# Kernel tuning notes

Measured on AMD Instinct MI355X. Metric: run time of the kernel, lower is better.

Reference implementation:

```python
import jax, jax.numpy as jnp
import numpy as np

N = 131072      # atoms
NB = 8192       # blocks (~16 atoms each)
H = 256         # hidden_size
NH = 8          # num_heads
HD = H // NH
RBF = 16
HQ = H // 4
CUTOFF = 10.0
EPS = 1e-5


def _ln(x, g, b):
    mu = jnp.mean(x, axis=-1, keepdims=True)
    var = jnp.var(x, axis=-1, keepdims=True)
    return (x - mu) * jax.lax.rsqrt(var + EPS) * g + b


def setup_inputs():
    key = jax.random.key(0)
    ks = jax.random.split(key, 20)
    w = lambda k, sh: jax.random.normal(k, sh, jnp.float32) * 0.02
    z = lambda d: jnp.zeros((d,), jnp.float32)
    return {
        'atom_features': jax.random.normal(ks[0], (N, H), jnp.float32),
        'atom_positions': jax.random.uniform(ks[1], (N, 3), jnp.float32) * 20.0,
        'block_id': jnp.arange(N, dtype=jnp.int32) // (N // NB),
        'inter_edges': jax.random.randint(ks[2], (2, 4 * NB), 0, NB, jnp.int32),
        'pma_seed': w(ks[3], (H,)),
        'pma_wq': w(ks[4], (H, H)), 'pma_bq': z(H),
        'pma_wk': w(ks[5], (H, H)), 'pma_bk': z(H),
        'pma_wv': w(ks[6], (H, H)), 'pma_bv': z(H),
        'pma_wo': w(ks[7], (H, H)), 'pma_bo': z(H),
        'centers': jnp.linspace(0.0, CUTOFF, RBF, dtype=jnp.float32),
        'widths': jnp.full((RBF,), CUTOFF / RBF, jnp.float32),
        'geom_w': w(ks[8], (RBF, HQ)), 'geom_b': z(HQ),
        'cq_w': w(ks[9], (H, H)), 'cq_b': z(H),
        'ck_w': w(ks[10], (H + HQ, H)), 'ck_b': z(H),
        'cv_w': w(ks[11], (H + HQ, H)), 'cv_b': z(H),
        'cmlp_w1': w(ks[12], (H, H)), 'cmlp_b1': z(H),
        'cmlp_w2': w(ks[13], (H, H)), 'cmlp_b2': z(H),
        'ffn_w1': w(ks[14], (H, 2 * H)), 'ffn_b1': z(2 * H),
        'ffn_w2': w(ks[15], (2 * H, H)), 'ffn_b2': z(H),
        'ln1_g': jnp.ones((H,), jnp.float32), 'ln1_b': z(H),
        'ln2_g': jnp.ones((H,), jnp.float32), 'ln2_b': z(H),
    }


def reference(atom_features, atom_positions, block_id, inter_edges,
              pma_seed, pma_wq, pma_bq, pma_wk, pma_bk, pma_wv, pma_bv, pma_wo, pma_bo,
              centers, widths, geom_w, geom_b, cq_w, cq_b, ck_w, ck_b, cv_w, cv_b,
              cmlp_w1, cmlp_b1, cmlp_w2, cmlp_b2, ffn_w1, ffn_b1, ffn_w2, ffn_b2,
              ln1_g, ln1_b, ln2_g, ln2_b):
    bid = block_id
    seg_sum = lambda x: jax.ops.segment_sum(x, bid, NB)
    seg_max = lambda x: jax.ops.segment_max(x, bid, NB)

    # --- VectorizedPMA: one learned query pools atoms -> block features (ragged segment attention) ---
    q = (pma_seed @ pma_wq + pma_bq).reshape(NH, HD)             # query shared by all blocks
    k = (atom_features @ pma_wk + pma_bk).reshape(N, NH, HD)
    v = (atom_features @ pma_wv + pma_bv).reshape(N, NH, HD)
    s = jnp.einsum('hd,nhd->nh', q, k) * (HD ** -0.5)            # [N, NH]
    e = jnp.exp(s - seg_max(s)[bid])
    wgt = e / jnp.maximum(seg_sum(e), 1e-20)[bid]
    block_feat = seg_sum(wgt[:, :, None] * v).reshape(NB, H) @ pma_wo + pma_bo  # [NB, H]

    # --- geometry: per-block centroid, relative distance, RBF encoding ---
    cnt = seg_sum(jnp.ones((N,), atom_positions.dtype))
    cent = seg_sum(atom_positions) / jnp.maximum(cnt, 1.0)[:, None]
    rel = atom_positions - cent[bid]
    dist = jnp.sqrt(jnp.sum(rel * rel, axis=1))
    rbf = jnp.exp(-((dist[:, None] - centers[None, :]) ** 2) / (2.0 * widths[None, :] ** 2))
    aug = jnp.concatenate([atom_features, rbf @ geom_w + geom_b], axis=1)       # [N, H+H/4]

    # --- block -> atoms cross attention (single query per block over its atoms) ---
    Q = block_feat @ cq_w + cq_b
    K = aug @ ck_w + ck_b
    V = aug @ cv_w + cv_b
    sc = jnp.sum(Q[bid] * K, axis=1) / float(np.sqrt(H))
    e2 = jnp.exp(sc - seg_max(sc)[bid])
    w2 = e2 / jnp.maximum(seg_sum(e2), 1e-20)[bid]
    ctx = seg_sum(w2[:, None] * V)                                # [NB, H]
    upd = jax.nn.relu(ctx @ cmlp_w1 + cmlp_b1) @ cmlp_w2 + cmlp_b2

    # --- broadcast update back to atoms, residual + LN, FFN + LN (eval: dropout = identity) ---
    x = _ln(atom_features + upd[bid], ln1_g, ln1_b)
    x = _ln(x + jax.nn.relu(x @ ffn_w1 + ffn_b1) @ ffn_w2 + ffn_b2, ln2_g, ln2_b)
    return x
```

## Files before the change

kernel.cpp:

```cpp
#include <hip/hip_runtime.h>
#include <hip/hip_bf16.h>

#define NATOMS 131072
#define NBLK   8192
#define HDIM   256
#define NHEAD  8
#define TDIM   336

typedef __attribute__((ext_vector_type(8))) short short8;
typedef __attribute__((ext_vector_type(4))) float floatx4;

__device__ __forceinline__ float bfu2f(unsigned short u) {
  unsigned int v = ((unsigned int)u) << 16;
  return __builtin_bit_cast(float, v);
}
__device__ __forceinline__ unsigned short f2bfu(float f) {
  unsigned int u = __builtin_bit_cast(unsigned int, f);
  u += 0x7fffu + ((u >> 16) & 1u);
  return (unsigned short)(u >> 16);
}
__device__ __forceinline__ unsigned int cvt2(float a, float b) {
  unsigned int r;
  asm("v_cvt_pk_bf16_f32 %0, %1, %2" : "=v"(r) : "v"(a), "v"(b));
  return r;
}

__global__ __launch_bounds__(352) void prepA(
    const float* __restrict__ seed, const float* __restrict__ Wq,
    const float* __restrict__ bq, const float* __restrict__ Wk,
    const float* __restrict__ bk, unsigned short* __restrict__ A_bfT,
    float* __restrict__ sb,
    const float* __restrict__ cq_w, const float* __restrict__ cq_b,
    const float* __restrict__ ck_w, const float* __restrict__ ck_b,
    float* __restrict__ M, float* __restrict__ vbias,
    const float* __restrict__ cv_w, const float* __restrict__ cv_b,
    const float* __restrict__ w1m, const float* __restrict__ b1m,
    unsigned short* __restrict__ CV1Tb, float* __restrict__ cb1,
    const float* __restrict__ fw1, const float* __restrict__ fw2,
    const float* __restrict__ w2m, const float* __restrict__ geom_w,
    unsigned short* __restrict__ W1t, unsigned short* __restrict__ W2t,
    unsigned short* __restrict__ W2mTb, unsigned short* __restrict__ geomT,
    const float* __restrict__ Wv, unsigned short* __restrict__ WvTb) {
  __shared__ float row[256];
  int t = threadIdx.x, b = blockIdx.x;
  if (b < 9) {
    if (t < 256) {
      float acc = bq[t];
      for (int c = 0; c < 256; ++c) acc += seed[c] * Wq[c * 256 + t];
      row[t] = acc;
    }
    __syncthreads();
    const float scale = 0.17677669529663687f;
    if (b < 8) {
      if (t < 256) {
        int o = b * 256 + t;
        int c = o >> 3, h = o & 7;
        float a = 0.f;
        for (int d = 0; d < 32; ++d) a += Wk[c * 256 + h * 32 + d] * row[h * 32 + d];
        A_bfT[h * 256 + c] = f2bfu(a * scale);
      }
    } else {
      if (t < 8) {
        float a = 0.f;
        for (int d = 0; d < 32; ++d) a += bk[t * 32 + d] * row[t * 32 + d];
        sb[t] = a * scale;
      }
      if (t < 256)
        for (int idx = t; idx < 2048; idx += 256) A_bfT[2048 + idx] = 0;
    }
  } else if (b < 265) {
    int i = b - 9;
    if (t < 256) row[t] = cq_w[i * 256 + t];
    __syncthreads();
    if (t < TDIM) {
      float a = 0.f;
      if (t < 320) { const float* w = ck_w + t * 256; for (int j = 0; j < 256; ++j) a += row[j] * w[j]; }
      else if (t == 320) { for (int j = 0; j < 256; ++j) a += row[j] * ck_b[j]; }
      M[i * TDIM + t] = a;
    }
    if (i == 0) {
      __syncthreads();
      if (t < 256) row[t] = cq_b[t];
      __syncthreads();
      if (t < TDIM) {
        float a = 0.f;
        if (t < 320) { const float* w = ck_w + t * 256; for (int j = 0; j < 256; ++j) a += row[j] * w[j]; }
        else if (t == 320) { for (int j = 0; j < 256; ++j) a += row[j] * ck_b[j]; }
        vbias[t] = a;
      }
    }
  } else if (b < 586) {
    int k = b - 265;
    if (t < 256) row[t] = (k < 320) ? cv_w[k * 256 + t] : cv_b[t];
    __syncthreads();
    if (t < 256) {
      float a = 0.f;
      for (int i = 0; i < 256; ++i) a += row[i] * w1m[i * 256 + t];
      if (k < 320) CV1Tb[t * 320 + k] = f2bfu(a);
      else cb1[t] = a + b1m[t];
    }
  } else if (b < 1611) {
    int bb = b - 586;
    if (bb < 512) {
      if (t < 256) W1t[bb * 256 + t] = f2bfu(fw1[t * 512 + bb]);
    } else if (bb < 768) {
      int n = bb - 512;
      if (t < 256)
        for (int m = 0; m < 2; ++m) {
          int k = t + 256 * m;
          W2t[n * 512 + k] = f2bfu(fw2[k * 256 + n]);
        }
    } else if (bb == 768) {
      if (t < 256)
        for (int idx = t; idx < 2048; idx += 256) {
          int q = idx >> 5, r = idx & 31;
          geomT[idx] = (r < 16) ? f2bfu(geom_w[r * 64 + q]) : (unsigned short)0;
        }
    } else {
      int n = bb - 769;
      if (t < 256) W2mTb[n * 256 + t] = f2bfu(w2m[t * 256 + n]);
    }
  } else {
    int j = b - 1611;
    if (t < 256) WvTb[j * 256 + t] = f2bfu(Wv[t * 256 + j]);
  }
}

__global__ __launch_bounds__(352) void kp2(const float* __restrict__ Wo,
    const float* __restrict__ bo, const float* __restrict__ M,
    const float* __restrict__ vbias, unsigned short* __restrict__ MMTb,
    float* __restrict__ vb2) {
  __shared__ float row[256];
  int p = blockIdx.x, t = threadIdx.x;
  const float* src = (p < 256) ? (Wo + p * 256) : bo;
  if (t < 256) row[t] = src[t];
  __syncthreads();
  if (t < TDIM) {
    float a = 0.f;
    for (int i = 0; i < 256; ++i) a += row[i] * M[i * TDIM + t];
    if (p < 256) MMTb[t * 256 + p] = f2bfu(a);
    else vb2[t] = a + vbias[t];
  }
}

__global__ __launch_bounds__(256, 4) void kgm(const float* __restrict__ x,
    const unsigned short* __restrict__ A_bfT, const float* __restrict__ sb,
    const unsigned short* __restrict__ WvTb, const float* __restrict__ bv,
    const unsigned short* __restrict__ MMTb, const float* __restrict__ vb2,
    float* __restrict__ T) {
  __shared__ __align__(16) char buf[33792];
  unsigned short (*xs)[264] = (unsigned short(*)[264])buf;
  unsigned short (*ysb)[8][264] = (unsigned short(*)[8][264])buf;
  __shared__ unsigned short wsm[64][8];
  __shared__ unsigned short bpb[4][264];
  int t = threadIdx.x, wg = blockIdx.x;
  long a0 = (long)wg * 64;
  int B0 = wg * 4;
  int lane = t & 63, w = t >> 6;
  int lrow = lane & 15, hi = lane >> 4, lk = hi * 8;

  const float4* x4 = (const float4*)(x + a0 * 256);
  for (int m = 0; m < 16; ++m) {
    int f4 = t + 256 * m;
    int row = f4 >> 6, c4 = f4 & 63;
    float4 v = x4[f4];
    uint2 q;
    q.x = cvt2(v.x, v.y);
    q.y = cvt2(v.z, v.w);
    *(uint2*)&xs[row][c4 * 4] = q;
  }
  float sblv = (lrow < 8) ? sb[lrow] : 0.f;
  __syncthreads();

  floatx4 zero = {0.f, 0.f, 0.f, 0.f};
  floatx4 accs = zero;
#pragma unroll
  for (int k0 = 0; k0 < 8; ++k0) {
    short8 af = *(const short8*)&xs[16 * w + lrow][k0 * 32 + lk];
    short8 bf = *(const short8*)(A_bfT + lrow * 256 + k0 * 32 + lk);
    accs = __builtin_amdgcn_mfma_f32_16x16x32_bf16(af, bf, accs, 0, 0, 0);
  }
  {
    float sv[4], e[4];
    float mx = -1e30f;
#pragma unroll
    for (int i = 0; i < 4; ++i) { sv[i] = accs[i] + sblv; mx = fmaxf(mx, sv[i]); }
    mx = fmaxf(mx, __shfl_xor(mx, 16));
    mx = fmaxf(mx, __shfl_xor(mx, 32));
    float se = 0.f;
#pragma unroll
    for (int i = 0; i < 4; ++i) { e[i] = __expf(sv[i] - mx); se += e[i]; }
    se += __shfl_xor(se, 16);
    se += __shfl_xor(se, 32);
    float inv = 1.f / fmaxf(se, 1e-20f);
    if (lrow < 8) {
#pragma unroll
      for (int i = 0; i < 4; ++i) wsm[16 * w + hi * 4 + i][lrow] = f2bfu(e[i] * inv);
    }
  }
  __syncthreads();

  int h = lrow & 7, bsel = lrow >> 3;
  short8 A1, A2;
#pragma unroll
  for (int j = 0; j < 8; ++j) {
    int atom = 8 * hi + j;
    unsigned short w1v = wsm[atom][h];
    unsigned short w2v = wsm[32 + atom][h];
    A1[j] = (bsel == (atom >> 4)) ? (short)w1v : (short)0;
    A2[j] = (bsel == (atom >> 4)) ? (short)w2v : (short)0;
  }
  floatx4 d1r[4], d2r[4];
#pragma unroll
  for (int q = 0; q < 4; ++q) {
    int ct = 4 * w + q;
    int cb = ct * 16 + lrow;
    short8 B1, B2;
#pragma unroll
    for (int j = 0; j < 8; ++j) {
      B1[j] = (short)xs[8 * hi + j][cb];
      B2[j] = (short)xs[32 + 8 * hi + j][cb];
    }
    d1r[q] = __builtin_amdgcn_mfma_f32_16x16x32_bf16(A1, B1, zero, 0, 0, 0);
    d2r[q] = __builtin_amdgcn_mfma_f32_16x16x32_bf16(A2, B2, zero, 0, 0, 0);
  }
  __syncthreads();

#pragma unroll
  for (int q = 0; q < 4; ++q) {
    int ct = 4 * w + q;
#pragma unroll
    for (int i = 0; i < 4; ++i) {
      int r = hi * 4 + i;
      int hh = r & 7, bb = r >> 3;
      ysb[bb][hh][ct * 16 + lrow] = f2bfu(d1r[q][i]);
      ysb[2 + bb][hh][ct * 16 + lrow] = f2bfu(d2r[q][i]);
    }
  }
  __syncthreads();

#pragma unroll
  for (int hh2 = 0; hh2 < 2; ++hh2) {
    int hd = 2 * w + hh2;
#pragma unroll
    for (int n = 0; n < 2; ++n) {
      floatx4 acc = zero;
#pragma unroll
      for (int ks = 0; ks < 8; ++ks) {
        short8 A = *(const short8*)&ysb[lrow & 3][hd][ks * 32 + lk];
        short8 B = *(const short8*)(WvTb + (hd * 32 + n * 16 + lrow) * 256 + ks * 32 + lk);
        acc = __builtin_amdgcn_mfma_f32_16x16x32_bf16(A, B, acc, 0, 0, 0);
      }
      if (hi == 0) {
        int col = hd * 32 + n * 16 + lrow;
        float bvc = bv[col];
#pragma unroll
        for (int i = 0; i < 4; ++i)
          bpb[i][col] = f2bfu(acc[i] + bvc);
      }
    }
  }
  __syncthreads();

  for (int ct = w; ct < 21; ct += 4) {
    floatx4 acc = zero;
#pragma unroll
    for (int ks = 0; ks < 8; ++ks) {
      short8 A = *(const short8*)&bpb[lrow & 3][ks * 32 + lk];
      short8 B = *(const short8*)(MMTb + (ct * 16 + lrow) * 256 + ks * 32 + lk);
      acc = __builtin_amdgcn_mfma_f32_16x16x32_bf16(A, B, acc, 0, 0, 0);
    }
    if (hi == 0) {
      int c = ct * 16 + lrow;
      float vb = vb2[c];
#pragma unroll
      for (int i = 0; i < 4; ++i)
        T[(long)(B0 + i) * TDIM + c] = acc[i] + vb;
    }
  }
}

__global__ __launch_bounds__(256) void kg3(const float* __restrict__ x,
    const float* __restrict__ pos, const float* __restrict__ T,
    const float* __restrict__ centers, const float* __restrict__ widths,
    const unsigned short* __restrict__ geomT, const float* __restrict__ geom_b,
    float* __restrict__ z_f) {
  __shared__ unsigned short xs[64][264];
  __shared__ unsigned short rbflb[64][32];
  __shared__ unsigned short rbfpb[64][72];
  __shared__ unsigned short TbfT[4][328];
  __shared__ float Tbias[4];
  __shared__ float ps[64][3];
  __shared__ float cent[4][3];
  __shared__ float ctr[16], wid[16];
  __shared__ float w2l[64];
  int t = threadIdx.x, wg = blockIdx.x;
  long a0 = (long)wg * 64;
  int b0 = wg * 4;
  int lane = t & 63, w = t >> 6;
  int lrow = lane & 15, hi = lane >> 4, lk = hi * 8;

  const float4* x4 = (const float4*)(x + a0 * 256);
  for (int m = 0; m < 16; ++m) {
    int f4 = t + 256 * m;
    int row = f4 >> 6, c4 = f4 & 63;
    float4 v = x4[f4];
    uint2 q;
    q.x = cvt2(v.x, v.y);
    q.y = cvt2(v.z, v.w);
    *(uint2*)&xs[row][c4 * 4] = q;
  }
  if (t < 192) ps[t / 3][t % 3] = pos[a0 * 3 + t];
  if (t >= 224 && t < 240) ctr[t - 224] = centers[t - 224];
  if (t >= 240) wid[t - 240] = widths[t - 240];
#pragma unroll
  for (int j = 0; j < 4; ++j)
    for (int c = t; c < 321; c += 256) {
      float v = T[(long)(b0 + j) * TDIM + c];
      if (c < 320) TbfT[j][c] = f2bfu(v);
      else Tbias[j] = v;
    }
  __syncthreads();
  if (t < 12) {
    int b = t / 3, d = t % 3;
    float s = 0.f;
    for (int i = 0; i < 16; ++i) s += ps[b * 16 + i][d];
    cent[b][d] = s * 0.0625f;
  }
  __syncthreads();
  if (t < 64) {
    int b = t >> 4;
    float dx = ps[t][0] - cent[b][0];
    float dy = ps[t][1] - cent[b][1];
    float dz = ps[t][2] - cent[b][2];
    float dist = sqrtf(dx * dx + dy * dy + dz * dz);
    for (int r = 0; r < 16; ++r) {
      float dd = dist - ctr[r];
      rbflb[t][r] = f2bfu(__expf(-dd * dd / (2.f * wid[r] * wid[r])));
      rbflb[t][16 + r] = 0;
    }
  }
  __syncthreads();

  floatx4 zero = {0.f, 0.f, 0.f, 0.f};
  {
    short8 A = *(const short8*)&rbflb[16 * w + lrow][lk];
#pragma unroll
    for (int qt = 0; qt < 4; ++qt) {
      short8 B = *(const short8*)(geomT + (qt * 16 + lrow) * 32 + lk);
      floatx4 d = __builtin_amdgcn_mfma_f32_16x16x32_bf16(A, B, zero, 0, 0, 0);
      float gb = geom_b[qt * 16 + lrow];
#pragma unroll
      for (int i = 0; i < 4; ++i)
        rbfpb[16 * w + hi * 4 + i][qt * 16 + lrow] = f2bfu(d[i] + gb);
    }
  }
  __syncthreads();

  {
    floatx4 acc = zero;
#pragma unroll
    for (int k0 = 0; k0 < 8; ++k0) {
      short8 af = *(const short8*)&xs[16 * w + lrow][k0 * 32 + lk];
      short8 bf = *(const short8*)&TbfT[lrow & 3][k0 * 32 + lk];
      acc = __builtin_amdgcn_mfma_f32_16x16x32_bf16(af, bf, acc, 0, 0, 0);
    }
#pragma unroll
    for (int kq = 0; kq < 2; ++kq) {
      short8 af = *(const short8*)&rbfpb[16 * w + lrow][kq * 32 + lk];
      short8 bf = *(const short8*)&TbfT[lrow & 3][256 + kq * 32 + lk];
      acc = __builtin_amdgcn_mfma_f32_16x16x32_bf16(af, bf, acc, 0, 0, 0);
    }
    float tb = Tbias[w];
    float sv[4], e[4];
    float mx = -1e30f;
#pragma unroll
    for (int i = 0; i < 4; ++i) { sv[i] = (acc[i] + tb) * 0.0625f; mx = fmaxf(mx, sv[i]); }
    mx = fmaxf(mx, __shfl_xor(mx, 16));
    mx = fmaxf(mx, __shfl_xor(mx, 32));
    float se = 0.f;
#pragma unroll
    for (int i = 0; i < 4; ++i) { e[i] = __expf(sv[i] - mx); se += e[i]; }
    se += __shfl_xor(se, 16);
    se += __shfl_xor(se, 32);
    float inv = 1.f / fmaxf(se, 1e-20f);
    if (lrow == w) {
#pragma unroll
      for (int i = 0; i < 4; ++i) w2l[16 * w + hi * 4 + i] = e[i] * inv;
    }
  }
  __syncthreads();

  for (int b = 0; b < 4; ++b) {
    float zv = 0.f;
    for (int i = 0; i < 16; ++i) zv += w2l[b * 16 + i] * bfu2f(xs[b * 16 + i][t]);
    z_f[(long)(b0 + b) * 320 + t] = zv;
  }
  {
    int q = t & 63, b = t >> 6;
    float zq = 0.f;
    for (int i = 0; i < 16; ++i) zq += w2l[b * 16 + i] * bfu2f(rbfpb[b * 16 + i][q]);
    z_f[(long)(b0 + b) * 320 + 256 + q] = zq;
  }
}

__global__ __launch_bounds__(256, 4) void gb2(const float* __restrict__ z_f,
    const unsigned short* __restrict__ CV1Tb, const float* __restrict__ cb1,
    const unsigned short* __restrict__ W2mTb, const float* __restrict__ b2m,
    float* __restrict__ upd) {
  __shared__ unsigned short zb[16][328];
  __shared__ unsigned short prb[16][264];
  int t = threadIdx.x;
  int B0 = blockIdx.x * 16;
  int lane = t & 63, w = t >> 6;
  int lrow = lane & 15, hi = lane >> 4, lk = hi * 8;
  floatx4 zero = {0.f, 0.f, 0.f, 0.f};

  for (int idx = t; idx < 16 * 320; idx += 256) {
    int r = idx / 320, c = idx - r * 320;
    zb[r][c] = f2bfu(z_f[(long)(B0 + r) * 320 + c]);
  }
  __syncthreads();

#pragma unroll
  for (int tt = 0; tt < 4; ++tt) {
    int colt = w * 4 + tt;
    floatx4 acc = zero;
    const unsigned short* ap = CV1Tb + (colt * 16 + lrow) * 320 + lk;
#pragma unroll
    for (int ks = 0; ks < 10; ++ks) {
      short8 A = *(const short8*)(ap + ks * 32);
      short8 B = *(const short8*)&zb[lrow][ks * 32 + lk];
      acc = __builtin_amdgcn_mfma_f32_16x16x32_bf16(A, B, acc, 0, 0, 0);
    }
    float4 cbv = ((const float4*)cb1)[colt * 4 + hi];
    float r0 = fmaxf(acc[0] + cbv.x, 0.f);
    float r1 = fmaxf(acc[1] + cbv.y, 0.f);
    float r2 = fmaxf(acc[2] + cbv.z, 0.f);
    float r3 = fmaxf(acc[3] + cbv.w, 0.f);
    uint2 q;
    q.x = cvt2(r0, r1);
    q.y = cvt2(r2, r3);
    *(uint2*)&prb[lrow][colt * 16 + hi * 4] = q;
  }
  __syncthreads();

#pragma unroll
  for (int tt = 0; tt < 4; ++tt) {
    int colt = w * 4 + tt;
    floatx4 acc = zero;
    const unsigned short* ap = W2mTb + (colt * 16 + lrow) * 256 + lk;
#pragma unroll
    for (int ks = 0; ks < 8; ++ks) {
      short8 A = *(const short8*)(ap + ks * 32);
      short8 B = *(const short8*)&prb[lrow][ks * 32 + lk];
      acc = __builtin_amdgcn_mfma_f32_16x16x32_bf16(A, B, acc, 0, 0, 0);
    }
    float4 b2v = ((const float4*)b2m)[colt * 4 + hi];
    float4 st;
    st.x = acc[0] + b2v.x;
    st.y = acc[1] + b2v.y;
    st.z = acc[2] + b2v.z;
    st.w = acc[3] + b2v.w;
    *(float4*)&upd[(long)(B0 + lrow) * 256 + colt * 16 + hi * 4] = st;
  }
}

__global__ __launch_bounds__(512, 4) void kf(const float* __restrict__ x,
    const float* __restrict__ upd, const unsigned short* __restrict__ W1t,
    const unsigned short* __restrict__ W2t, const float* __restrict__ b1,
    const float* __restrict__ b2, const float* __restrict__ g1,
    const float* __restrict__ be1, const float* __restrict__ g2,
    const float* __restrict__ be2, float* __restrict__ out) {
  __shared__ unsigned short x1s[64][264];
  __shared__ unsigned short hs[64][136];
  int t = threadIdx.x, wg = blockIdx.x;
  long a0 = (long)wg * 64;
  int b0 = wg * 4;
  int lane = t & 63, w = t >> 6;
  int lrow = lane & 15, hi = lane >> 4;
  int lk = hi * 8;

  {
    float4 gv1 = ((const float4*)g1)[lane];
    float4 bv1 = ((const float4*)be1)[lane];
#pragma unroll
    for (int rr = 0; rr < 8; ++rr) {
      int row = w * 8 + rr;
      float4 xv = ((const float4*)(x + (a0 + row) * 256))[lane];
      float4 uv = ((const float4*)(upd + (long)(b0 + (row >> 4)) * 256))[lane];
      float4 v;
      v.x = xv.x + uv.x; v.y = xv.y + uv.y; v.z = xv.z + uv.z; v.w = xv.w + uv.w;
      float s = v.x + v.y + v.z + v.w;
      float sq = v.x * v.x + v.y * v.y + v.z * v.z + v.w * v.w;
#pragma unroll
      for (int d = 1; d < 64; d <<= 1) { s += __shfl_xor(s, d); sq += __shfl_xor(sq, d); }
      float mu = s * (1.f / 256.f);
      float var = sq * (1.f / 256.f) - mu * mu;
      float rstd = rsqrtf(fmaxf(var, 0.f) + 1e-5f);
      uint2 q;
      q.x = cvt2((v.x - mu) * rstd * gv1.x + bv1.x, (v.y - mu) * rstd * gv1.y + bv1.y);
      q.y = cvt2((v.z - mu) * rstd * gv1.z + bv1.z, (v.w - mu) * rstd * gv1.w + bv1.w);
      *(uint2*)&x1s[row][lane * 4] = q;
    }
  }
  __syncthreads();

  floatx4 zero = {0.f, 0.f, 0.f, 0.f};
  floatx4 acc2[2][4];
#pragma unroll
  for (int cb = 0; cb < 2; ++cb)
    for (int rb = 0; rb < 4; ++rb) acc2[cb][rb] = zero;

  for (int s = 0; s < 4; ++s) {
    int hc = s * 128 + w * 16 + lrow;
    short8 wf[8];
#pragma unroll
    for (int k0 = 0; k0 < 8; ++k0)
      wf[k0] = *(const short8*)(W1t + hc * 256 + k0 * 32 + lk);
    floatx4 acc1[4] = {zero, zero, zero, zero};
#pragma unroll
    for (int k0 = 0; k0 < 8; ++k0) {
      short8 af0 = *(const short8*)&x1s[0 + lrow][k0 * 32 + lk];
      short8 af1 = *(const short8*)&x1s[16 + lrow][k0 * 32 + lk];
      short8 af2 = *(const short8*)&x1s[32 + lrow][k0 * 32 + lk];
      short8 af3 = *(const short8*)&x1s[48 + lrow][k0 * 32 + lk];
      acc1[0] = __builtin_amdgcn_mfma_f32_16x16x32_bf16(wf[k0], af0, acc1[0], 0, 0, 0);
      acc1[1] = __builtin_amdgcn_mfma_f32_16x16x32_bf16(wf[k0], af1, acc1[1], 0, 0, 0);
      acc1[2] = __builtin_amdgcn_mfma_f32_16x16x32_bf16(wf[k0], af2, acc1[2], 0, 0, 0);
      acc1[3] = __builtin_amdgcn_mfma_f32_16x16x32_bf16(wf[k0], af3, acc1[3], 0, 0, 0);
    }
    short8 wf2[8];
#pragma unroll
    for (int cb = 0; cb < 2; ++cb)
      for (int ks = 0; ks < 4; ++ks)
        wf2[cb * 4 + ks] = *(const short8*)(W2t + (w * 32 + cb * 16 + lrow) * 512 + s * 128 + ks * 32 + lk);
    float4 b4 = ((const float4*)b1)[s * 32 + w * 4 + hi];
    __syncthreads();
#pragma unroll
    for (int rb = 0; rb < 4; ++rb) {
      float r0 = fmaxf(acc1[rb][0] + b4.x, 0.f);
      float r1 = fmaxf(acc1[rb][1] + b4.y, 0.f);
      float r2 = fmaxf(acc1[rb][2] + b4.z, 0.f);
      float r3 = fmaxf(acc1[rb][3] + b4.w, 0.f);
      uint2 q;
      q.x = cvt2(r0, r1);
      q.y = cvt2(r2, r3);
      *(uint2*)&hs[rb * 16 + lrow][w * 16 + hi * 4] = q;
    }
    __syncthreads();
#pragma unroll
    for (int ks = 0; ks < 4; ++ks) {
      short8 a20 = *(const short8*)&hs[0 + lrow][ks * 32 + lk];
      short8 a21 = *(const short8*)&hs[16 + lrow][ks * 32 + lk];
      short8 a22 = *(const short8*)&hs[32 + lrow][ks * 32 + lk];
      short8 a23 = *(const short8*)&hs[48 + lrow][ks * 32 + lk];
#pragma unroll
      for (int cb = 0; cb < 2; ++cb) {
        acc2[cb][0] = __builtin_amdgcn_mfma_f32_16x16x32_bf16(wf2[cb * 4 + ks], a20, acc2[cb][0], 0, 0, 0);
        acc2[cb][1] = __builtin_amdgcn_mfma_f32_16x16x32_bf16(wf2[cb * 4 + ks], a21, acc2[cb][1], 0, 0, 0);
        acc2[cb][2] = __builtin_amdgcn_mfma_f32_16x16x32_bf16(wf2[cb * 4 + ks], a22, acc2[cb][2], 0, 0, 0);
        acc2[cb][3] = __builtin_amdgcn_mfma_f32_16x16x32_bf16(wf2[cb * 4 + ks], a23, acc2[cb][3], 0, 0, 0);
      }
    }
  }

#pragma unroll
  for (int cb = 0; cb < 2; ++cb) {
    float4 b4 = ((const float4*)b2)[w * 8 + cb * 4 + hi];
    int colb = w * 32 + cb * 16 + hi * 4;
#pragma unroll
    for (int rb = 0; rb < 4; ++rb) {
      int atom = rb * 16 + lrow;
      ushort4 old = *(const ushort4*)&x1s[atom][colb];
      float r0 = acc2[cb][rb][0] + b4.x + bfu2f(old.x);
      float r1 = acc2[cb][rb][1] + b4.y + bfu2f(old.y);
      float r2 = acc2[cb][rb][2] + b4.z + bfu2f(old.z);
      float r3 = acc2[cb][rb][3] + b4.w + bfu2f(old.w);
      uint2 q;
      q.x = cvt2(r0, r1);
      q.y = cvt2(r2, r3);
      *(uint2*)&x1s[atom][colb] = q;
    }
  }
  __syncthreads();

  {
    float4 gv2 = ((const float4*)g2)[lane];
    float4 bv2 = ((const float4*)be2)[lane];
#pragma unroll
    for (int rr = 0; rr < 8; ++rr) {
      int row = w * 8 + rr;
      ushort4 u = *(const ushort4*)&x1s[row][lane * 4];
      float v0 = bfu2f(u.x), v1 = bfu2f(u.y), v2 = bfu2f(u.z), v3 = bfu2f(u.w);
      float s = v0 + v1 + v2 + v3;
      float sq = v0 * v0 + v1 * v1 + v2 * v2 + v3 * v3;
#pragma unroll
      for (int d = 1; d < 64; d <<= 1) { s += __shfl_xor(s, d); sq += __shfl_xor(sq, d); }
      float mu = s * (1.f / 256.f);
      float var = sq * (1.f / 256.f) - mu * mu;
      float rstd = rsqrtf(fmaxf(var, 0.f) + 1e-5f);
      float4 o;
      o.x = (v0 - mu) * rstd * gv2.x + bv2.x;
      o.y = (v1 - mu) * rstd * gv2.y + bv2.y;
      o.z = (v2 - mu) * rstd * gv2.z + bv2.z;
      o.w = (v3 - mu) * rstd * gv2.w + bv2.w;
      ((float4*)(out + (a0 + row) * 256))[lane] = o;
    }
  }
}

extern "C" void kernel_launch(void* const* d_in, const int* in_sizes, int n_in,
                              void* d_out, int out_size, void* d_ws, size_t ws_size,
                              hipStream_t stream) {
  (void)in_sizes; (void)n_in; (void)out_size; (void)ws_size;
  const float* x    = (const float*)d_in[0];
  const float* pos  = (const float*)d_in[1];
  const float* seed = (const float*)d_in[4];
  const float* Wq   = (const float*)d_in[5];
  const float* bq   = (const float*)d_in[6];
  const float* Wk   = (const float*)d_in[7];
  const float* bk   = (const float*)d_in[8];
  const float* Wv   = (const float*)d_in[9];
  const float* bv   = (const float*)d_in[10];
  const float* Wo   = (const float*)d_in[11];
  const float* bo   = (const float*)d_in[12];
  const float* centers = (const float*)d_in[13];
  const float* widths  = (const float*)d_in[14];
  const float* geom_w  = (const float*)d_in[15];
  const float* geom_b  = (const float*)d_in[16];
  const float* cq_w = (const float*)d_in[17];
  const float* cq_b = (const float*)d_in[18];
  const float* ck_w = (const float*)d_in[19];
  const float* ck_b = (const float*)d_in[20];
  const float* cv_w = (const float*)d_in[21];
  const float* cv_b = (const float*)d_in[22];
  const float* w1m  = (const float*)d_in[23];
  const float* b1m  = (const float*)d_in[24];
  const float* w2m  = (const float*)d_in[25];
  const float* b2m  = (const float*)d_in[26];
  const float* fw1  = (const float*)d_in[27];
  const float* fb1  = (const float*)d_in[28];
  const float* fw2  = (const float*)d_in[29];
  const float* fb2  = (const float*)d_in[30];
  const float* g1   = (const float*)d_in[31];
  const float* be1  = (const float*)d_in[32];
  const float* g2   = (const float*)d_in[33];
  const float* be2  = (const float*)d_in[34];

  float* ws = (float*)d_ws;
  float* sb = ws + 0;
  unsigned short* A_bfT = (unsigned short*)(ws + 64);
  float* M     = ws + 2112;
  float* vbias = ws + 88128;
  unsigned short* MMTb = (unsigned short*)(ws + 88480);
  float* vb2   = ws + 131488;
  unsigned short* CV1Tb = (unsigned short*)(ws + 131840);
  float* cb1   = ws + 172800;
  unsigned short* W1t = (unsigned short*)(ws + 173056);
  unsigned short* W2t = (unsigned short*)(ws + 238592);
  unsigned short* W2mTb = (unsigned short*)(ws + 304128);
  unsigned short* WvTb = (unsigned short*)(ws + 336896);
  float* updw = ws + 369664;
  unsigned short* geomT = (unsigned short*)(ws + 2466816);

  float* outp = (float*)d_out;
  float* T   = outp + 16777216;
  float* zf  = outp + 21626880;

  prepA<<<dim3(1867), dim3(352), 0, stream>>>(seed, Wq, bq, Wk, bk, A_bfT, sb,
      cq_w, cq_b, ck_w, ck_b, M, vbias,
      cv_w, cv_b, w1m, b1m, CV1Tb, cb1,
      fw1, fw2, w2m, geom_w, W1t, W2t, W2mTb, geomT, Wv, WvTb);
  kp2<<<dim3(257), dim3(352), 0, stream>>>(Wo, bo, M, vbias, MMTb, vb2);
  kgm<<<dim3(2048), dim3(256), 0, stream>>>(x, A_bfT, sb, WvTb, bv, MMTb, vb2, T);
  kg3<<<dim3(2048), dim3(256), 0, stream>>>(x, pos, T, centers, widths, geomT, geom_b, zf);
  gb2<<<dim3(512), dim3(256), 0, stream>>>(zf, CV1Tb, cb1, W2mTb, b2m, updw);
  kf<<<dim3(2048), dim3(512), 0, stream>>>(x, updw, W1t, W2t, fb1, fb2, g1, be1, g2, be2, outp);
}
```

Baseline: 335.3 us.

## Fuse PMA block-query kernel with geometry/cross-attention kernel

Merges the kgm kernel, which computes the per-block PMA output and T, into kg3 so that T stays in shared memory as bf16 and is never written to or read back from global memory. It also removes one launch and the second load and bf16 conversion of the same 64-atom x tile. In exchange the fused kernel uses more shared memory, aliasing ysb with rbfpb, and drops the occupancy hint of 4 blocks per CU, which may reduce concurrency.

```diff
diff --git a/kernel.cpp b/kernel.cpp
--- a/kernel.cpp
+++ b/kernel.cpp
@@ -143,21 +143,34 @@
   }
 }
 
-__global__ __launch_bounds__(256, 4) void kgm(const float* __restrict__ x,
+__global__ __launch_bounds__(256) void kgm3(const float* __restrict__ x,
+    const float* __restrict__ pos,
     const unsigned short* __restrict__ A_bfT, const float* __restrict__ sb,
     const unsigned short* __restrict__ WvTb, const float* __restrict__ bv,
     const unsigned short* __restrict__ MMTb, const float* __restrict__ vb2,
-    float* __restrict__ T) {
-  __shared__ __align__(16) char buf[33792];
-  unsigned short (*xs)[264] = (unsigned short(*)[264])buf;
-  unsigned short (*ysb)[8][264] = (unsigned short(*)[8][264])buf;
+    const float* __restrict__ centers, const float* __restrict__ widths,
+    const unsigned short* __restrict__ geomT, const float* __restrict__ geom_b,
+    float* __restrict__ z_f) {
+  __shared__ unsigned short xs[64][264];
+  __shared__ __align__(16) char r2[16896];
+  unsigned short (*ysb)[8][264] = (unsigned short(*)[8][264])r2;
+  unsigned short (*rbfpb)[72] = (unsigned short(*)[72])r2;
+  __shared__ unsigned short rbflb[64][32];
+  __shared__ unsigned short bpb[4][264];
+  __shared__ unsigned short TbfT[4][328];
+  __shared__ float Tbias[4];
   __shared__ unsigned short wsm[64][8];
-  __shared__ unsigned short bpb[4][264];
+  __shared__ float ps[64][3];
+  __shared__ float cent[4][3];
+  __shared__ float ctr[16], wid[16];
+  __shared__ float w2l[64];
+
   int t = threadIdx.x, wg = blockIdx.x;
   long a0 = (long)wg * 64;
-  int B0 = wg * 4;
+  int b0 = wg * 4;
   int lane = t & 63, w = t >> 6;
   int lrow = lane & 15, hi = lane >> 4, lk = hi * 8;
+  floatx4 zero = {0.f, 0.f, 0.f, 0.f};
 
   const float4* x4 = (const float4*)(x + a0 * 256);
   for (int m = 0; m < 16; ++m) {
@@ -169,158 +182,12 @@
     q.y = cvt2(v.z, v.w);
     *(uint2*)&xs[row][c4 * 4] = q;
   }
-  float sblv = (lrow < 8) ? sb[lrow] : 0.f;
-  __syncthreads();
-
-  floatx4 zero = {0.f, 0.f, 0.f, 0.f};
-  floatx4 accs = zero;
-#pragma unroll
-  for (int k0 = 0; k0 < 8; ++k0) {
-    short8 af = *(const short8*)&xs[16 * w + lrow][k0 * 32 + lk];
-    short8 bf = *(const short8*)(A_bfT + lrow * 256 + k0 * 32 + lk);
-    accs = __builtin_amdgcn_mfma_f32_16x16x32_bf16(af, bf, accs, 0, 0, 0);
-  }
-  {
-    float sv[4], e[4];
-    float mx = -1e30f;
-#pragma unroll
-    for (int i = 0; i < 4; ++i) { sv[i] = accs[i] + sblv; mx = fmaxf(mx, sv[i]); }
-    mx = fmaxf(mx, __shfl_xor(mx, 16));
-    mx = fmaxf(mx, __shfl_xor(mx, 32));
-    float se = 0.f;
-#pragma unroll
-    for (int i = 0; i < 4; ++i) { e[i] = __expf(sv[i] - mx); se += e[i]; }
-    se += __shfl_xor(se, 16);
-    se += __shfl_xor(se, 32);
-    float inv = 1.f / fmaxf(se, 1e-20f);
-    if (lrow < 8) {
-#pragma unroll
-      for (int i = 0; i < 4; ++i) wsm[16 * w + hi * 4 + i][lrow] = f2bfu(e[i] * inv);
-    }
-  }
-  __syncthreads();
-
-  int h = lrow & 7, bsel = lrow >> 3;
-  short8 A1, A2;
-#pragma unroll
-  for (int j = 0; j < 8; ++j) {
-    int atom = 8 * hi + j;
-    unsigned short w1v = wsm[atom][h];
-    unsigned short w2v = wsm[32 + atom][h];
-    A1[j] = (bsel == (atom >> 4)) ? (short)w1v : (short)0;
-    A2[j] = (bsel == (atom >> 4)) ? (short)w2v : (short)0;
-  }
-  floatx4 d1r[4], d2r[4];
-#pragma unroll
-  for (int q = 0; q < 4; ++q) {
-    int ct = 4 * w + q;
-    int cb = ct * 16 + lrow;
-    short8 B1, B2;
-#pragma unroll
-    for (int j = 0; j < 8; ++j) {
-      B1[j] = (short)xs[8 * hi + j][cb];
-      B2[j] = (short)xs[32 + 8 * hi + j][cb];
-    }
-    d1r[q] = __builtin_amdgcn_mfma_f32_16x16x32_bf16(A1, B1, zero, 0, 0, 0);
-    d2r[q] = __builtin_amdgcn_mfma_f32_16x16x32_bf16(A2, B2, zero, 0, 0, 0);
-  }
-  __syncthreads();
-
-#pragma unroll
-  for (int q = 0; q < 4; ++q) {
-    int ct = 4 * w + q;
-#pragma unroll
-    for (int i = 0; i < 4; ++i) {
-      int r = hi * 4 + i;
-      int hh = r & 7, bb = r >> 3;
-      ysb[bb][hh][ct * 16 + lrow] = f2bfu(d1r[q][i]);
-      ysb[2 + bb][hh][ct * 16 + lrow] = f2bfu(d2r[q][i]);
-    }
-  }
-  __syncthreads();
-
-#pragma unroll
-  for (int hh2 = 0; hh2 < 2; ++hh2) {
-    int hd = 2 * w + hh2;
-#pragma unroll
-    for (int n = 0; n < 2; ++n) {
-      floatx4 acc = zero;
-#pragma unroll
-      for (int ks = 0; ks < 8; ++ks) {
-        short8 A = *(const short8*)&ysb[lrow & 3][hd][ks * 32 + lk];
-        short8 B = *(const short8*)(WvTb + (hd * 32 + n * 16 + lrow) * 256 + ks * 32 + lk);
-        acc = __builtin_amdgcn_mfma_f32_16x16x32_bf16(A, B, acc, 0, 0, 0);
-      }
-      if (hi == 0) {
-        int col = hd * 32 + n * 16 + lrow;
-        float bvc = bv[col];
-#pragma unroll
-        for (int i = 0; i < 4; ++i)
-          bpb[i][col] = f2bfu(acc[i] + bvc);
-      }
-    }
-  }
-  __syncthreads();
-
-  for (int ct = w; ct < 21; ct += 4) {
-    floatx4 acc = zero;
-#pragma unroll
-    for (int ks = 0; ks < 8; ++ks) {
-      short8 A = *(const short8*)&bpb[lrow & 3][ks * 32 + lk];
-      short8 B = *(const short8*)(MMTb + (ct * 16 + lrow) * 256 + ks * 32 + lk);
-      acc = __builtin_amdgcn_mfma_f32_16x16x32_bf16(A, B, acc, 0, 0, 0);
-    }
-    if (hi == 0) {
-      int c = ct * 16 + lrow;
-      float vb = vb2[c];
-#pragma unroll
-      for (int i = 0; i < 4; ++i)
-        T[(long)(B0 + i) * TDIM + c] = acc[i] + vb;
-    }
-  }
-}
-
-__global__ __launch_bounds__(256) void kg3(const float* __restrict__ x,
-    const float* __restrict__ pos, const float* __restrict__ T,
-    const float* __restrict__ centers, const float* __restrict__ widths,
-    const unsigned short* __restrict__ geomT, const float* __restrict__ geom_b,
-    float* __restrict__ z_f) {
-  __shared__ unsigned short xs[64][264];
-  __shared__ unsigned short rbflb[64][32];
-  __shared__ unsigned short rbfpb[64][72];
-  __shared__ unsigned short TbfT[4][328];
-  __shared__ float Tbias[4];
-  __shared__ float ps[64][3];
-  __shared__ float cent[4][3];
-  __shared__ float ctr[16], wid[16];
-  __shared__ float w2l[64];
-  int t = threadIdx.x, wg = blockIdx.x;
-  long a0 = (long)wg * 64;
-  int b0 = wg * 4;
-  int lane = t & 63, w = t >> 6;
-  int lrow = lane & 15, hi = lane >> 4, lk = hi * 8;
-
-  const float4* x4 = (const float4*)(x + a0 * 256);
-  for (int m = 0; m < 16; ++m) {
-    int f4 = t + 256 * m;
-    int row = f4 >> 6, c4 = f4 & 63;
-    float4 v = x4[f4];
-    uint2 q;
-    q.x = cvt2(v.x, v.y);
-    q.y = cvt2(v.z, v.w);
-    *(uint2*)&xs[row][c4 * 4] = q;
-  }
   if (t < 192) ps[t / 3][t % 3] = pos[a0 * 3 + t];
   if (t >= 224 && t < 240) ctr[t - 224] = centers[t - 224];
   if (t >= 240) wid[t - 240] = widths[t - 240];
-#pragma unroll
-  for (int j = 0; j < 4; ++j)
-    for (int c = t; c < 321; c += 256) {
-      float v = T[(long)(b0 + j) * TDIM + c];
-      if (c < 320) TbfT[j][c] = f2bfu(v);
-      else Tbias[j] = v;
-    }
-  __syncthreads();
+  float sblv = (lrow < 8) ? sb[lrow] : 0.f;
+  __syncthreads();
+
   if (t < 12) {
     int b = t / 3, d = t % 3;
     float s = 0.f;
@@ -328,6 +195,7 @@
     cent[b][d] = s * 0.0625f;
   }
   __syncthreads();
+
   if (t < 64) {
     int b = t >> 4;
     float dx = ps[t][0] - cent[b][0];
@@ -340,9 +208,91 @@
       rbflb[t][16 + r] = 0;
     }
   }
-  __syncthreads();
-
-  floatx4 zero = {0.f, 0.f, 0.f, 0.f};
+
+  {
+    floatx4 accs = zero;
+#pragma unroll
+    for (int k0 = 0; k0 < 8; ++k0) {
+      short8 af = *(const short8*)&xs[16 * w + lrow][k0 * 32 + lk];
+      short8 bf = *(const short8*)(A_bfT + lrow * 256 + k0 * 32 + lk);
+      accs = __builtin_amdgcn_mfma_f32_16x16x32_bf16(af, bf, accs, 0, 0, 0);
+    }
+    float sv[4], e[4];
+    float mx = -1e30f;
+#pragma unroll
+    for (int i = 0; i < 4; ++i) { sv[i] = accs[i] + sblv; mx = fmaxf(mx, sv[i]); }
+    mx = fmaxf(mx, __shfl_xor(mx, 16));
+    mx = fmaxf(mx, __shfl_xor(mx, 32));
+    float se = 0.f;
+#pragma unroll
+    for (int i = 0; i < 4; ++i) { e[i] = __expf(sv[i] - mx); se += e[i]; }
+    se += __shfl_xor(se, 16);
+    se += __shfl_xor(se, 32);
+    float inv = 1.f / fmaxf(se, 1e-20f);
+    if (lrow < 8) {
+#pragma unroll
+      for (int i = 0; i < 4; ++i) wsm[16 * w + hi * 4 + i][lrow] = f2bfu(e[i] * inv);
+    }
+  }
+  __syncthreads();
+
+  {
+    int h = lrow & 7, bsel = lrow >> 3;
+    short8 A1, A2;
+#pragma unroll
+    for (int j = 0; j < 8; ++j) {
+      int atom = 8 * hi + j;
+      unsigned short w1v = wsm[atom][h];
+      unsigned short w2v = wsm[32 + atom][h];
+      A1[j] = (bsel == (atom >> 4)) ? (short)w1v : (short)0;
+      A2[j] = (bsel == (atom >> 4)) ? (short)w2v : (short)0;
+    }
+#pragma unroll
+    for (int q = 0; q < 4; ++q) {
+      int ct = 4 * w + q;
+      int cb = ct * 16 + lrow;
+      short8 B1, B2;
+#pragma unroll
+      for (int j = 0; j < 8; ++j) {
+        B1[j] = (short)xs[8 * hi + j][cb];
+        B2[j] = (short)xs[32 + 8 * hi + j][cb];
+      }
+      floatx4 d1 = __builtin_amdgcn_mfma_f32_16x16x32_bf16(A1, B1, zero, 0, 0, 0);
+      floatx4 d2 = __builtin_amdgcn_mfma_f32_16x16x32_bf16(A2, B2, zero, 0, 0, 0);
+#pragma unroll
+      for (int i = 0; i < 4; ++i) {
+        int r = hi * 4 + i;
+        int hh = r & 7, bb = r >> 3;
+        ysb[bb][hh][ct * 16 + lrow] = f2bfu(d1[i]);
+        ysb[2 + bb][hh][ct * 16 + lrow] = f2bfu(d2[i]);
+      }
+    }
+  }
+  __syncthreads();
+
+#pragma unroll
+  for (int hh2 = 0; hh2 < 2; ++hh2) {
+    int hd = 2 * w + hh2;
+#pragma unroll
+    for (int n = 0; n < 2; ++n) {
+      floatx4 acc = zero;
+#pragma unroll
+      for (int ks = 0; ks < 8; ++ks) {
+        short8 A = *(const short8*)&ysb[lrow & 3][hd][ks * 32 + lk];
+        short8 B = *(const short8*)(WvTb + (hd * 32 + n * 16 + lrow) * 256 + ks * 32 + lk);
+        acc = __builtin_amdgcn_mfma_f32_16x16x32_bf16(A, B, acc, 0, 0, 0);
+      }
+      if (hi == 0) {
+        int col = hd * 32 + n * 16 + lrow;
+        float bvc = bv[col];
+#pragma unroll
+        for (int i = 0; i < 4; ++i)
+          bpb[i][col] = f2bfu(acc[i] + bvc);
+      }
+    }
+  }
+  __syncthreads();
+
   {
     short8 A = *(const short8*)&rbflb[16 * w + lrow][lk];
 #pragma unroll
@@ -353,6 +303,28 @@
 #pragma unroll
       for (int i = 0; i < 4; ++i)
         rbfpb[16 * w + hi * 4 + i][qt * 16 + lrow] = f2bfu(d[i] + gb);
+    }
+  }
+  for (int ct = w; ct < 21; ct += 4) {
+    floatx4 acc = zero;
+#pragma unroll
+    for (int ks = 0; ks < 8; ++ks) {
+      short8 A = *(const short8*)&bpb[lrow & 3][ks * 32 + lk];
+      short8 B = *(const short8*)(MMTb + (ct * 16 + lrow) * 256 + ks * 32 + lk);
+      acc = __builtin_amdgcn_mfma_f32_16x16x32_bf16(A, B, acc, 0, 0, 0);
+    }
+    if (hi == 0) {
+      int c = ct * 16 + lrow;
+      if (c <= 320) {
+        float vb = vb2[c];
+        if (c < 320) {
+#pragma unroll
+          for (int i = 0; i < 4; ++i) TbfT[i][c] = f2bfu(acc[i] + vb);
+        } else {
+#pragma unroll
+          for (int i = 0; i < 4; ++i) Tbias[i] = acc[i] + vb;
+        }
+      }
     }
   }
   __syncthreads();
@@ -665,7 +637,6 @@
   unsigned short* geomT = (unsigned short*)(ws + 2466816);
 
   float* outp = (float*)d_out;
-  float* T   = outp + 16777216;
   float* zf  = outp + 21626880;
 
   prepA<<<dim3(1867), dim3(352), 0, stream>>>(seed, Wq, bq, Wk, bk, A_bfT, sb,
@@ -673,8 +644,8 @@
       cv_w, cv_b, w1m, b1m, CV1Tb, cb1,
       fw1, fw2, w2m, geom_w, W1t, W2t, W2mTb, geomT, Wv, WvTb);
   kp2<<<dim3(257), dim3(352), 0, stream>>>(Wo, bo, M, vbias, MMTb, vb2);
-  kgm<<<dim3(2048), dim3(256), 0, stream>>>(x, A_bfT, sb, WvTb, bv, MMTb, vb2, T);
-  kg3<<<dim3(2048), dim3(256), 0, stream>>>(x, pos, T, centers, widths, geomT, geom_b, zf);
+  kgm3<<<dim3(2048), dim3(256), 0, stream>>>(x, pos, A_bfT, sb, WvTb, bv, MMTb, vb2,
+      centers, widths, geomT, geom_b, zf);
   gb2<<<dim3(512), dim3(256), 0, stream>>>(zf, CV1Tb, cb1, W2mTb, b2m, updw);
   kf<<<dim3(2048), dim3(512), 0, stream>>>(x, updw, W1t, W2t, fb1, fb2, g1, be1, g2, be2, outp);
 }
```

Result: faster. 321.7 us (-4.1%).
